# Kernel optimization log

Measured on AMD Instinct MI355X. Metric: run time of the kernel, lower is better.

## Reference

```python
import jax, jax.numpy as jnp
import numpy as np


def setup_inputs() -> dict:
    key = jax.random.key(0)
    k1, k2, k3, k4, k5 = jax.random.split(key, 5)
    B, C, H, W = 4, 256, 64, 64
    INTER = 128
    # NOTE: original inits out.weight to zeros (residual identity at init);
    # we use small random weights so the reference exercises the full math.
    s = 0.02
    return {
        "x": jax.random.normal(k1, (B, C, H, W), dtype=jnp.float32),
        "w_theta": jax.random.normal(k2, (INTER, C), dtype=jnp.float32) * s,
        "w_phi": jax.random.normal(k3, (INTER, C), dtype=jnp.float32) * s,
        "w_g": jax.random.normal(k4, (INTER, C), dtype=jnp.float32) * s,
        "w_out": jax.random.normal(k5, (C, INTER), dtype=jnp.float32) * s,
    }


def reference(x, w_theta, w_phi, w_g, w_out):
    B, C, H, W = x.shape
    N = H * W
    xf = x.reshape(B, C, N)                      # [B, C, N]
    theta = jnp.einsum("ic,bcn->bni", w_theta, xf)  # [B, N, inter]
    phi = jnp.einsum("ic,bcn->bin", w_phi, xf)      # [B, inter, N]
    g = jnp.einsum("ic,bcn->bni", w_g, xf)          # [B, N, inter]
    attn = jax.nn.softmax(jnp.einsum("bni,bim->bnm", theta, phi), axis=-1)  # [B, N, N]
    y = jnp.einsum("bnm,bmi->bin", attn, g)         # [B, inter, N]
    out = jnp.einsum("ci,bin->bcn", w_out, y)       # [B, C, N]
    return x + out.reshape(B, C, H, W)
```

## Files before the change

### kernel.cpp

```cpp
#include <hip/hip_runtime.h>
#include <hip/hip_bf16.h>
#include <cstdint>

#define BATCH 4
#define CDIM 256
#define NTOK 4096
#define IDIM 128

typedef __attribute__((ext_vector_type(4))) float f32x4;
typedef __attribute__((ext_vector_type(16))) float f32x16;
typedef __attribute__((ext_vector_type(8))) short short8;

static __device__ __forceinline__ unsigned cvt_pk(float lo, float hi) {
  unsigned r;
  asm("v_cvt_pk_bf16_f32 %0, %1, %2" : "=v"(r) : "v"(lo), "v"(hi));
  return r;
}
static __device__ __forceinline__ float bf2f(unsigned short u) {
  union { unsigned u; float f; } v;
  v.u = (unsigned)u << 16;
  return v.f;
}
static __device__ __forceinline__ float exp2_f(float x) {
#if __has_builtin(__builtin_amdgcn_exp2f)
  return __builtin_amdgcn_exp2f(x);
#else
  return exp2f(x);
#endif
}
static __device__ __forceinline__ void gl16(const void* g, void* l) {
  __builtin_amdgcn_global_load_lds(
      (const __attribute__((address_space(1))) void*)g,
      (__attribute__((address_space(3))) void*)l, 16, 0, 0);
}

__global__ __launch_bounds__(256) void cast_w_kernel(
    const float* __restrict__ wt, const float* __restrict__ wp,
    const float* __restrict__ wg, const float* __restrict__ wo,
    unsigned short* __restrict__ Wb)
{
  int id = blockIdx.x * 256 + threadIdx.x;
  if (id < 24576) {
    int pidx = id >> 13;
    int rem = id & 8191;
    int i = rem >> 6, c4 = (rem & 63) * 4;
    const float* src = pidx == 0 ? wt : pidx == 1 ? wp : wg;
    float4 v = *(const float4*)&src[i * 256 + c4];
    float s = (pidx == 0) ? 1.4426950408889634f : 1.0f;
    uint2 u = make_uint2(cvt_pk(v.x * s, v.y * s), cvt_pk(v.z * s, v.w * s));
    *(uint2*)&Wb[(((size_t)pidx * 32 + (c4 >> 3)) * 128 + i) * 8 + (c4 & 7)] = u;
  } else {
    int rem = id - 24576;
    int c = rem >> 5, i4 = (rem & 31) * 4;
    float4 v = *(const float4*)&wo[c * 128 + i4];
    uint2 u = make_uint2(cvt_pk(v.x, v.y), cvt_pk(v.z, v.w));
    *(uint2*)&Wb[98304 + (((size_t)(i4 >> 3) * 256 + c) * 8) + (i4 & 7)] = u;
  }
}

__global__ __launch_bounds__(768) void qkv_kernel(
    const float* __restrict__ x, const unsigned short* __restrict__ Wb,
    unsigned short* __restrict__ Q, unsigned short* __restrict__ K,
    unsigned short* __restrict__ Vt)
{
  __shared__ __align__(16) unsigned short xt[64 * 256];
  __shared__ __align__(16) unsigned short sc[8][16 * 128];

  const int b = blockIdx.y;
  const int n0 = blockIdx.x * 64;
  const int t = threadIdx.x;
  const float* xb = x + (size_t)b * CDIM * NTOK;

  for (int it = 0; it < 3; ++it) {
    int u = it * 768 + t;
    if (u < 2048) {
      int c0 = (u >> 4) * 2;
      int n4 = (u & 15) * 4;
      float4 va = *(const float4*)&xb[(size_t)c0 * NTOK + n0 + n4];
      float4 vb = *(const float4*)&xb[(size_t)(c0 + 1) * NTOK + n0 + n4];
      const float* pa = (const float*)&va;
      const float* pb = (const float*)&vb;
#pragma unroll
      for (int j = 0; j < 4; ++j) {
        int n = n4 + j;
        unsigned pk = cvt_pk(pa[j], pb[j]);
        *(unsigned*)((char*)xt + n * 512 + ((c0 * 2) ^ ((n & 15) << 4))) = pk;
      }
    }
  }
  __syncthreads();

  const int lane = t & 63;
  const int wv = __builtin_amdgcn_readfirstlane(t >> 6);
  const int nsub = wv & 3, proj = wv >> 2;
  const int cl = lane & 15, g = lane >> 4;

  f32x4 acc[8];
#pragma unroll
  for (int i = 0; i < 8; ++i) acc[i] = (f32x4){0.f, 0.f, 0.f, 0.f};

  const int nrow = nsub * 16 + cl;
  const int swz = (nrow & 15) << 4;
#pragma unroll
  for (int kc = 0; kc < 8; ++kc) {
    int cb = kc * 32 + g * 8;
    short8 af = *(const short8*)((const char*)xt + nrow * 512 + ((cb * 2) ^ swz));
#pragma unroll
    for (int is = 0; is < 8; ++is) {
      short8 bf = *(const short8*)&Wb[(((size_t)proj * 32 + kc * 4 + g) * 128 +
                                       is * 16 + cl) * 8];
      acc[is] = __builtin_amdgcn_mfma_f32_16x16x32_bf16(af, bf, acc[is], 0, 0, 0);
    }
  }

  if (proj < 2) {
    unsigned short* scw = sc[wv];
#pragma unroll
    for (int is = 0; is < 8; ++is)
#pragma unroll
      for (int r = 0; r < 4; ++r) {
        int nl = g * 4 + r;
        int i2 = (is * 16 + cl) * 2;
        *(unsigned short*)((char*)scw + nl * 256 + (i2 ^ ((nl & 15) << 4))) =
            (unsigned short)cvt_pk(acc[is][r], 0.f);
      }
    unsigned short* dst = (proj == 0 ? Q : K) +
        ((size_t)b * NTOK + n0 + nsub * 16) * IDIM;
    int nr = lane >> 2;
    int swr = (nr & 15) << 4;
#pragma unroll
    for (int j = 0; j < 4; ++j) {
      int ch = (lane & 3) + 4 * j;
      short8 v = *(const short8*)((const char*)scw + nr * 256 + ((ch * 16) ^ swr));
      *(short8*)&dst[(size_t)nr * IDIM + ch * 8] = v;
    }
  } else {
    unsigned short* dstV = Vt + (size_t)b * IDIM * NTOK + n0 + nsub * 16 + g * 4;
#pragma unroll
    for (int is = 0; is < 8; ++is) {
      uint2 u = make_uint2(cvt_pk(acc[is][0], acc[is][1]),
                           cvt_pk(acc[is][2], acc[is][3]));
      *(uint2*)&dstV[(size_t)(is * 16 + cl) * NTOK] = u;
    }
  }
}

__global__ __launch_bounds__(128, 2) void attn_kernel(
    const unsigned short* __restrict__ Q, const unsigned short* __restrict__ K,
    const unsigned short* __restrict__ Vt, unsigned short* __restrict__ Op,
    float2* __restrict__ ML)
{
  __shared__ __align__(16) unsigned short kls[2][32 * 128];
  __shared__ __align__(16) unsigned short vls[2][128 * 32];

  const int bid = blockIdx.x;
  const int b = (bid >> 1) & 3;
  const int ms = (bid >> 3) & 3;
  const int nblk = (bid >> 5) + (bid & 1) * 32;
  const int t = threadIdx.x;
  const int lane = t & 63;
  const int wv = __builtin_amdgcn_readfirstlane(t >> 6);
  const int n0 = nblk * 64 + wv * 32;
  const int c32 = lane & 31, hl = lane >> 5;
  const int p = t;

  const unsigned short* Kb = K + (size_t)b * NTOK * IDIM;
  const unsigned short* Vb = Vt + (size_t)b * IDIM * NTOK;

  const unsigned short* Qp = Q + ((size_t)b * NTOK + n0 + c32) * IDIM + hl * 8;
  short8 q[8];
#pragma unroll
  for (int kc = 0; kc < 8; ++kc) q[kc] = *(const short8*)(Qp + kc * 16);

  int koff[8];
#pragma unroll
  for (int kc = 0; kc < 8; ++kc)
    koff[kc] = c32 * 256 + ((((kc * 2 + hl) ^ (c32 & 7))) << 4);
  int voff[8];
#pragma unroll
  for (int it = 0; it < 4; ++it)
#pragma unroll
    for (int kt = 0; kt < 2; ++kt) {
      int rp = it * 16 + (c32 >> 1);
      voff[it * 2 + kt] =
          rp * 128 + ((((c32 & 1) * 4 + kt * 2 + hl) ^ (rp & 7)) << 4);
    }
  int kgo[4], vgo[4], lofs[4];
#pragma unroll
  for (int u = 0; u < 4; ++u) {
    int idx = p + 128 * u;
    lofs[u] = idx * 16;
    int r = idx >> 4, ch = idx & 15;
    kgo[u] = r * IDIM + ((ch ^ (r & 7)) * 8);
    int rp = idx >> 3, pp = idx & 7;
    int s = pp ^ (rp & 7);
    vgo[u] = (rp * 2 + (s >> 2)) * NTOK + (s & 3) * 8;
  }

  f32x16 o[4];
#pragma unroll
  for (int it = 0; it < 4; ++it)
#pragma unroll
    for (int e = 0; e < 16; ++e) o[it][e] = 0.f;
  float M = -3.0e38f, L = 0.f;

#define STAGE(cb, m0_)                                                        \
  {                                                                           \
    const unsigned short* Kit = Kb + (size_t)(m0_)*IDIM;                      \
    const unsigned short* Vit = Vb + (m0_);                                   \
    _Pragma("unroll")                                                         \
    for (int u = 0; u < 4; ++u)                                               \
      gl16(Kit + kgo[u], (char*)kls[cb] + lofs[u]);                           \
    _Pragma("unroll")                                                         \
    for (int u = 0; u < 4; ++u)                                               \
      gl16(Vit + vgo[u], (char*)vls[cb] + lofs[u]);                           \
  }

  const int mbase = ms * 1024;
  STAGE(0, mbase)

  for (int tt = 0; tt < 32; ++tt) {
    asm volatile("s_waitcnt vmcnt(0) lgkmcnt(0)\n\ts_barrier" ::: "memory");
    if (tt < 31) STAGE((tt + 1) & 1, mbase + (tt + 1) * 32)

    const char* kbuf = (const char*)kls[tt & 1];
    const char* vbuf = (const char*)vls[tt & 1];

    f32x16 sa, sb;
#pragma unroll
    for (int e = 0; e < 16; ++e) { sa[e] = 0.f; sb[e] = 0.f; }
    __builtin_amdgcn_s_setprio(1);
#pragma unroll
    for (int kc = 0; kc < 4; ++kc) {
      short8 ka = *(const short8*)(kbuf + koff[kc]);
      short8 kb2 = *(const short8*)(kbuf + koff[kc + 4]);
      sa = __builtin_amdgcn_mfma_f32_32x32x16_bf16(ka, q[kc], sa, 0, 0, 0);
      sb = __builtin_amdgcn_mfma_f32_32x32x16_bf16(kb2, q[kc + 4], sb, 0, 0, 0);
    }
    __builtin_amdgcn_s_setprio(0);
    f32x16 st = sa + sb;

    float mx[8];
#pragma unroll
    for (int j = 0; j < 8; ++j) mx[j] = fmaxf(st[j], st[j + 8]);
#pragma unroll
    for (int j = 0; j < 4; ++j) mx[j] = fmaxf(mx[j], mx[j + 4]);
    float sm = fmaxf(fmaxf(mx[0], mx[1]), fmaxf(mx[2], mx[3]));
    sm = fmaxf(sm, __shfl_xor(sm, 32));
    if (!__all(sm <= M + 11.5f)) {
      float Mn = fmaxf(M, sm);
      float scl = exp2_f(M - Mn);
      M = Mn;
      L *= scl;
#pragma unroll
      for (int it = 0; it < 4; ++it)
#pragma unroll
        for (int e = 0; e < 16; ++e) o[it][e] *= scl;
    }
    float pr[16];
#pragma unroll
    for (int e = 0; e < 16; ++e) pr[e] = exp2_f(st[e] - M);
    float sv[8];
#pragma unroll
    for (int j = 0; j < 8; ++j) sv[j] = pr[j] + pr[j + 8];
#pragma unroll
    for (int j = 0; j < 4; ++j) sv[j] += sv[j + 4];
    float ls = (sv[0] + sv[1]) + (sv[2] + sv[3]);
    ls += __shfl_xor(ls, 32);
    L += ls;

    short8 pf[2];
#pragma unroll
    for (int kt = 0; kt < 2; ++kt) {
      unsigned a0 = cvt_pk(pr[kt * 8 + 0], pr[kt * 8 + 1]);
      unsigned a1 = cvt_pk(pr[kt * 8 + 2], pr[kt * 8 + 3]);
      unsigned a2 = cvt_pk(pr[kt * 8 + 4], pr[kt * 8 + 5]);
      unsigned a3 = cvt_pk(pr[kt * 8 + 6], pr[kt * 8 + 7]);
      asm volatile("v_permlane32_swap_b32 %0, %1" : "+v"(a0), "+v"(a2));
      asm volatile("v_permlane32_swap_b32 %0, %1" : "+v"(a1), "+v"(a3));
      union { unsigned u[4]; short8 s; } w;
      w.u[0] = a0; w.u[1] = a1; w.u[2] = a2; w.u[3] = a3;
      pf[kt] = w.s;
    }

    __builtin_amdgcn_s_setprio(1);
#pragma unroll
    for (int it = 0; it < 4; ++it) {
#pragma unroll
      for (int kt = 0; kt < 2; ++kt) {
        short8 vf = *(const short8*)(vbuf + voff[it * 2 + kt]);
        o[it] = __builtin_amdgcn_mfma_f32_32x32x16_bf16(vf, pf[kt], o[it], 0, 0, 0);
      }
    }
    __builtin_amdgcn_s_setprio(0);
  }
#undef STAGE

  {
    const int sb2 = ms * 4 + b;
    unsigned short* Ob = Op + (size_t)sb2 * (16 * NTOK * 8);
#pragma unroll
    for (int it = 0; it < 4; ++it)
#pragma unroll
      for (int g2 = 0; g2 < 4; ++g2) {
        uint2 u2 = make_uint2(cvt_pk(o[it][4 * g2 + 0], o[it][4 * g2 + 1]),
                              cvt_pk(o[it][4 * g2 + 2], o[it][4 * g2 + 3]));
        *(uint2*)&Ob[((size_t)(it * 4 + g2) * NTOK + n0 + c32) * 8 + 4 * hl] = u2;
      }
    if (hl == 0) ML[(size_t)sb2 * NTOK + n0 + c32] = make_float2(M, L);
  }
}

__global__ __launch_bounds__(256) void out_kernel(
    const float* __restrict__ x, const unsigned short* __restrict__ Wb,
    const unsigned short* __restrict__ Op, const float2* __restrict__ ML,
    float* __restrict__ out)
{
  const int b = blockIdx.y;
  const int n0 = blockIdx.x * 32;
  const int t = threadIdx.x;
  const int lane = t & 63;
  const int wv = __builtin_amdgcn_readfirstlane(t >> 6);
  const int cl = lane & 15, g = lane >> 4;

  float ws4[2][4];
#pragma unroll
  for (int nsb = 0; nsb < 2; ++nsb) {
    int n = n0 + nsb * 16 + cl;
    float2 m0 = ML[(size_t)(0 * 4 + b) * NTOK + n];
    float2 m1 = ML[(size_t)(1 * 4 + b) * NTOK + n];
    float2 m2 = ML[(size_t)(2 * 4 + b) * NTOK + n];
    float2 m3 = ML[(size_t)(3 * 4 + b) * NTOK + n];
    float Mx = fmaxf(fmaxf(m0.x, m1.x), fmaxf(m2.x, m3.x));
    float w0 = exp2_f(m0.x - Mx), w1 = exp2_f(m1.x - Mx);
    float w2 = exp2_f(m2.x - Mx), w3 = exp2_f(m3.x - Mx);
    float rinv = 1.f / (w0 * m0.y + w1 * m1.y + w2 * m2.y + w3 * m3.y);
    ws4[nsb][0] = w0 * rinv; ws4[nsb][1] = w1 * rinv;
    ws4[nsb][2] = w2 * rinv; ws4[nsb][3] = w3 * rinv;
  }

  f32x4 acc[4][2];
#pragma unroll
  for (int cs = 0; cs < 4; ++cs)
#pragma unroll
    for (int nsb = 0; nsb < 2; ++nsb) acc[cs][nsb] = (f32x4){0.f, 0.f, 0.f, 0.f};

#pragma unroll
  for (int kc = 0; kc < 4; ++kc) {
    short8 bf[2];
#pragma unroll
    for (int nsb = 0; nsb < 2; ++nsb) {
      int n = n0 + nsb * 16 + cl;
      size_t base = ((size_t)(kc * 4 + g) * NTOK + n) * 8;
      const short8 f0 = *(const short8*)&Op[(size_t)(0 * 4 + b) * (16 * NTOK * 8) + base];
      const short8 f1 = *(const short8*)&Op[(size_t)(1 * 4 + b) * (16 * NTOK * 8) + base];
      const short8 f2 = *(const short8*)&Op[(size_t)(2 * 4 + b) * (16 * NTOK * 8) + base];
      const short8 f3 = *(const short8*)&Op[(size_t)(3 * 4 + b) * (16 * NTOK * 8) + base];
      float a[8];
#pragma unroll
      for (int e = 0; e < 8; ++e)
        a[e] = ws4[nsb][0] * bf2f((unsigned short)f0[e]) +
               ws4[nsb][1] * bf2f((unsigned short)f1[e]) +
               ws4[nsb][2] * bf2f((unsigned short)f2[e]) +
               ws4[nsb][3] * bf2f((unsigned short)f3[e]);
      union { unsigned u[4]; short8 s; } r;
#pragma unroll
      for (int jp = 0; jp < 4; ++jp) r.u[jp] = cvt_pk(a[2 * jp], a[2 * jp + 1]);
      bf[nsb] = r.s;
    }
#pragma unroll
    for (int cs = 0; cs < 4; ++cs) {
      short8 af = *(const short8*)&Wb[98304 +
          (((size_t)(kc * 4 + g)) * 256 + wv * 64 + cs * 16 + cl) * 8];
#pragma unroll
      for (int nsb = 0; nsb < 2; ++nsb)
        acc[cs][nsb] = __builtin_amdgcn_mfma_f32_16x16x32_bf16(af, bf[nsb], acc[cs][nsb], 0, 0, 0);
    }
  }

  const float* xb = x + (size_t)b * CDIM * NTOK;
  float* ob = out + (size_t)b * CDIM * NTOK;
#pragma unroll
  for (int cs = 0; cs < 4; ++cs)
#pragma unroll
    for (int nsb = 0; nsb < 2; ++nsb)
#pragma unroll
      for (int r = 0; r < 4; ++r) {
        int c = wv * 64 + cs * 16 + g * 4 + r;
        int n = n0 + nsb * 16 + cl;
        ob[(size_t)c * NTOK + n] = xb[(size_t)c * NTOK + n] + acc[cs][nsb][r];
      }
}

extern "C" void kernel_launch(void* const* d_in, const int* in_sizes, int n_in,
                              void* d_out, int out_size, void* d_ws, size_t ws_size,
                              hipStream_t stream) {
  const float* x  = (const float*)d_in[0];
  const float* wt = (const float*)d_in[1];
  const float* wp = (const float*)d_in[2];
  const float* wg = (const float*)d_in[3];
  const float* wo = (const float*)d_in[4];
  float* outp = (float*)d_out;

  char* ws = (char*)d_ws;
  unsigned short* Wb  = (unsigned short*)(ws);
  unsigned short* Qd  = (unsigned short*)(ws + (size_t)1  * (1 << 20));
  unsigned short* Kd  = (unsigned short*)(ws + (size_t)5  * (1 << 20));
  unsigned short* Vtd = (unsigned short*)(ws + (size_t)9  * (1 << 20));
  unsigned short* Opd = (unsigned short*)(ws + (size_t)13 * (1 << 20));
  float2* MLd         = (float2*)(ws + (size_t)29 * (1 << 20));

  cast_w_kernel<<<128, 256, 0, stream>>>(wt, wp, wg, wo, Wb);
  qkv_kernel<<<dim3(64, BATCH), 768, 0, stream>>>(x, Wb, Qd, Kd, Vtd);
  attn_kernel<<<1024, 128, 0, stream>>>(Qd, Kd, Vtd, Opd, MLd);
  out_kernel<<<dim3(128, BATCH), 256, 0, stream>>>(x, Wb, Opd, MLd, outp);
}
```

Before: 80.92 us.

## Triple-buffer K tiles and split K/V staging with partial vmcnt waits

Splits the combined K/V tile staging into separate K and V loads. K becomes triple-buffered and is prefetched two iterations ahead, while V stays double-buffered one iteration ahead. The single full drain before each iteration is replaced by partial vmcnt waits plus barriers before the QK and PV phases, so global loads can stay in flight across iterations. This adds LDS use, which may affect occupancy at 2 blocks per SM, an extra barrier per iteration, and redundant loads of the last tile at the loop tail.

```diff
diff --git a/kernel.cpp b/kernel.cpp
--- a/kernel.cpp
+++ b/kernel.cpp
@@ -150,7 +150,7 @@
     const unsigned short* __restrict__ Vt, unsigned short* __restrict__ Op,
     float2* __restrict__ ML)
 {
-  __shared__ __align__(16) unsigned short kls[2][32 * 128];
+  __shared__ __align__(16) unsigned short kls[3][32 * 128];
   __shared__ __align__(16) unsigned short vls[2][128 * 32];
 
   const int bid = blockIdx.x;
@@ -159,8 +159,7 @@
   const int nblk = (bid >> 5) + (bid & 1) * 32;
   const int t = threadIdx.x;
   const int lane = t & 63;
-  const int wv = __builtin_amdgcn_readfirstlane(t >> 6);
-  const int n0 = nblk * 64 + wv * 32;
+  const int n0 = nblk * 64 + ((t >> 6) << 5);
   const int c32 = lane & 31, hl = lane >> 5;
   const int p = t;
 
@@ -204,27 +203,42 @@
     for (int e = 0; e < 16; ++e) o[it][e] = 0.f;
   float M = -3.0e38f, L = 0.f;
 
-#define STAGE(cb, m0_)                                                        \
+#define STAGE_K(cb, m0_)                                                      \
   {                                                                           \
     const unsigned short* Kit = Kb + (size_t)(m0_)*IDIM;                      \
+    _Pragma("unroll")                                                         \
+    for (int u = 0; u < 4; ++u)                                               \
+      gl16(Kit + kgo[u], (char*)kls[cb] + lofs[u]);                           \
+  }
+#define STAGE_V(cb, m0_)                                                      \
+  {                                                                           \
     const unsigned short* Vit = Vb + (m0_);                                   \
     _Pragma("unroll")                                                         \
     for (int u = 0; u < 4; ++u)                                               \
-      gl16(Kit + kgo[u], (char*)kls[cb] + lofs[u]);                           \
-    _Pragma("unroll")                                                         \
-    for (int u = 0; u < 4; ++u)                                               \
       gl16(Vit + vgo[u], (char*)vls[cb] + lofs[u]);                           \
   }
 
   const int mbase = ms * 1024;
-  STAGE(0, mbase)
+  asm volatile("s_waitcnt vmcnt(0)" ::: "memory");
+  STAGE_K(0, mbase)
+  STAGE_V(0, mbase)
+  STAGE_K(1, mbase + 32)
+
+  int kr = 0;
+  int vr = 0;
 
   for (int tt = 0; tt < 32; ++tt) {
-    asm volatile("s_waitcnt vmcnt(0) lgkmcnt(0)\n\ts_barrier" ::: "memory");
-    if (tt < 31) STAGE((tt + 1) & 1, mbase + (tt + 1) * 32)
-
-    const char* kbuf = (const char*)kls[tt & 1];
-    const char* vbuf = (const char*)vls[tt & 1];
+    asm volatile("s_waitcnt vmcnt(8)\n\ts_barrier" ::: "memory");
+    {
+      int mv = mbase + (tt >= 31 ? 31 : tt + 1) * 32;
+      int mk = mbase + (tt >= 30 ? 31 : tt + 2) * 32;
+      STAGE_V(vr ^ 1, mv)
+      STAGE_K(kr == 0 ? 2 : kr - 1, mk)
+      __builtin_amdgcn_sched_barrier(0);
+    }
+
+    const char* kbuf = (const char*)kls[kr];
+    const char* vbuf = (const char*)vls[vr];
 
     f32x16 sa, sb;
 #pragma unroll
@@ -283,6 +297,8 @@
       pf[kt] = w.s;
     }
 
+    asm volatile("s_waitcnt vmcnt(12)\n\ts_barrier" ::: "memory");
+
     __builtin_amdgcn_s_setprio(1);
 #pragma unroll
     for (int it = 0; it < 4; ++it) {
@@ -293,8 +309,12 @@
       }
     }
     __builtin_amdgcn_s_setprio(0);
-  }
-#undef STAGE
+
+    kr = (kr == 2) ? 0 : kr + 1;
+    vr ^= 1;
+  }
+#undef STAGE_K
+#undef STAGE_V
 
   {
     const int sb2 = ms * 4 + b;
```

After: 81.02 us. About the same (+0.1%).
